# Optimization experiments

Measured on AMD Instinct MI355X. Metric: run time of the kernel, lower is better.

The kernel has to match this reference:

```python
import math
import jax, jax.numpy as jnp
import numpy as np

HEAD_DIM = 128
SKETCH_DIM = 256  # multiple of 8, no padding needed in pack
_BIT_WEIGHTS = jnp.array([1, 2, 4, 8, 16, 32, 64, 128], dtype=jnp.uint8)


def _pack_bits(bits):
    # bits: uint8 0/1, trailing dim = SKETCH_DIM (multiple of 8)
    *lead, d = bits.shape
    b = bits.reshape(*lead, d // 8, 8)
    return (b * _BIT_WEIGHTS).sum(axis=-1).astype(jnp.uint8)


def _unpack_bits(packed, out_dim):
    # packed: uint8 [..., n] -> float32 [..., out_dim] of 0/1
    shifts = jnp.arange(8, dtype=jnp.uint8)
    bits = (packed[..., None] >> shifts) & jnp.uint8(1)
    bits = bits.reshape(*packed.shape[:-1], -1)[..., :out_dim]
    return bits.astype(jnp.float32)


def setup_inputs() -> dict:
    key = jax.random.key(0)
    kq, kk, kg = jax.random.split(key, 3)
    q = jax.random.normal(kq, (4, 32, 16, HEAD_DIM), dtype=jnp.float32)
    k = jax.random.normal(kk, (4, 32, 8192, HEAD_DIM), dtype=jnp.float32)
    G = jax.random.normal(kg, (HEAD_DIM, SKETCH_DIM), dtype=jnp.float32) / math.sqrt(SKETCH_DIM)
    return {"q": q, "k": k, "G": G}


def reference(q, k, G):
    # project_query: q @ G -> [B, H, Q, sketch_dim]
    q_sketch = jnp.einsum('bhqd,ds->bhqs', q, G)
    # sketch_key: sign-quantize k @ G, pack into uint8
    proj = jnp.einsum('bhkd,ds->bhks', k, G)
    bits = (proj > 0).astype(jnp.uint8)
    k_packed = _pack_bits(bits)  # [B, H, K, sketch_dim//8] uint8
    # estimate_scores: unpack to +/-1, dequant matmul, unbiasing scale
    k_signs = _unpack_bits(k_packed, SKETCH_DIM) * 2.0 - 1.0
    est = jnp.einsum('bhqs,bhks->bhqk', q_sketch, k_signs.astype(q_sketch.dtype))
    return est * jnp.float32(math.sqrt(math.pi / 2))
```

## Files before the change

### kernel.cpp

```cpp
#include <hip/hip_runtime.h>
#include <math.h>

typedef _Float16 f16;
typedef _Float16 f16x4 __attribute__((ext_vector_type(4)));
typedef _Float16 f16x8 __attribute__((ext_vector_type(8)));
typedef float    f32x4 __attribute__((ext_vector_type(4)));
typedef unsigned int u32;
typedef unsigned long long u64;

#define NHEADS 128
#define KLEN   8192
#define DDIM   128
#define SDIM   256
#define NROWS  (NHEADS * KLEN)
#define SCALE  1.2533141373155003f
#define TAU    2e-5f

#define QS_OFF     0
#define GFH_OFF    (1u << 20)
#define GFL_OFF    ((1u << 20) + (64u << 10))
#define GT_OFF     ((1u << 20) + (128u << 10))
#define PACKED_OFF (2u << 20)

__device__ __forceinline__ float seq_dot_np(const float* __restrict__ a,
                                            const float* __restrict__ gcol) {
  float acc = 0.0f;
  #pragma unroll 8
  for (int d = 0; d < DDIM; ++d)
    acc = __builtin_fmaf(a[d], gcol[d], acc);
  return acc;
}

__global__ void prep_qs_kernel(const float* __restrict__ q,
                               const float* __restrict__ G,
                               f16* __restrict__ qs16) {
  int idx = blockIdx.x * 256 + threadIdx.x;
  int s  = idx & 255;
  int hq = idx >> 8;
  const float* qr = q + (size_t)hq * DDIM;
  float acc = 0.f;
  #pragma unroll 8
  for (int d = 0; d < DDIM; ++d) acc += qr[d] * G[d * SDIM + s];
  qs16[idx] = (f16)acc;
}

__global__ void prep_g_kernel(const float* __restrict__ G,
                              f16* __restrict__ gfh, f16* __restrict__ gfl,
                              float* __restrict__ gt) {
  int t = blockIdx.x * 256 + threadIdx.x;
  int tl   = t >> 8;
  int c    = (t >> 6) & 3;
  int lane = t & 63;
  int s  = tl * 16 + (lane & 15);
  int d0 = c * 32 + (lane >> 4) * 8;
  f16x8 hh, ll;
  #pragma unroll
  for (int j = 0; j < 8; ++j) {
    float g = G[(size_t)(d0 + j) * SDIM + s];
    f16 h = (f16)g;
    hh[j] = h;
    ll[j] = (f16)((g - (float)h) * 4096.0f);
    gt[(size_t)s * DDIM + d0 + j] = g;
  }
  *(f16x8*)(gfh + (size_t)t * 8) = hh;
  *(f16x8*)(gfl + (size_t)t * 8) = ll;
}

__launch_bounds__(512, 1)
__global__ void proj_sign_kernel(const float* __restrict__ kmat,
                                 const f16* __restrict__ gfh,
                                 const f16* __restrict__ gfl,
                                 u32* __restrict__ packed,
                                 u32* __restrict__ smask) {
  __shared__ __align__(16) f16 lds[2][4][64][8];

  const int tid  = threadIdx.x;
  const int lane = tid & 63;
  const int w    = tid >> 6;
  const int g4 = lane >> 4;
  const int ln = lane & 15;
  const size_t rowbase = (size_t)blockIdx.x * 256;

  f16x8 Gh[2][4], Gl[2][4];
  #pragma unroll
  for (int mt = 0; mt < 2; ++mt)
    #pragma unroll
    for (int kc = 0; kc < 4; ++kc) {
      size_t o = ((size_t)((w * 2 + mt) * 4 + kc) * 64 + lane) * 8;
      Gh[mt][kc] = *(const f16x8*)(gfh + o);
      Gl[mt][kc] = *(const f16x8*)(gfl + o);
    }

  const int srl = tid >> 5;
  const int sd0 = (tid & 31) * 4;
  const int skc = sd0 >> 5;
  const int slf = srl | (((sd0 >> 3) & 3) << 4);
  const int sj0 = sd0 & 7;

  float4 rv = *(const float4*)(kmat + (rowbase + srl) * DDIM + sd0);

  for (int t = 0; t < 16; ++t) {
    f16x4 h4, l4;
    {
      float vv0 = rv.x, vv1 = rv.y, vv2 = rv.z, vv3 = rv.w;
      f16 h;
      h = (f16)vv0; h4[0] = h; l4[0] = (f16)((vv0 - (float)h) * 4096.0f);
      h = (f16)vv1; h4[1] = h; l4[1] = (f16)((vv1 - (float)h) * 4096.0f);
      h = (f16)vv2; h4[2] = h; l4[2] = (f16)((vv2 - (float)h) * 4096.0f);
      h = (f16)vv3; h4[3] = h; l4[3] = (f16)((vv3 - (float)h) * 4096.0f);
    }
    float4 rn;
    if (t < 15)
      rn = *(const float4*)(kmat + (rowbase + (size_t)(t + 1) * 16 + srl) * DDIM + sd0);
    *(f16x4*)&lds[0][skc][slf][sj0] = h4;
    *(f16x4*)&lds[1][skc][slf][sj0] = l4;
    __syncthreads();

    f32x4 ah0 = {0,0,0,0}, aa0 = {0,0,0,0}, ab0 = {0,0,0,0};
    f32x4 ah1 = {0,0,0,0}, aa1 = {0,0,0,0}, ab1 = {0,0,0,0};
    #pragma unroll
    for (int kc = 0; kc < 4; ++kc) {
      f16x8 Bh = *(const f16x8*)&lds[0][kc][lane][0];
      f16x8 Bl = *(const f16x8*)&lds[1][kc][lane][0];
      ah0 = __builtin_amdgcn_mfma_f32_16x16x32_f16(Gh[0][kc], Bh, ah0, 0, 0, 0);
      aa0 = __builtin_amdgcn_mfma_f32_16x16x32_f16(Gh[0][kc], Bl, aa0, 0, 0, 0);
      ab0 = __builtin_amdgcn_mfma_f32_16x16x32_f16(Gl[0][kc], Bh, ab0, 0, 0, 0);
      ah1 = __builtin_amdgcn_mfma_f32_16x16x32_f16(Gh[1][kc], Bh, ah1, 0, 0, 0);
      aa1 = __builtin_amdgcn_mfma_f32_16x16x32_f16(Gh[1][kc], Bl, aa1, 0, 0, 0);
      ab1 = __builtin_amdgcn_mfma_f32_16x16x32_f16(Gl[1][kc], Bh, ab1, 0, 0, 0);
    }
    float p[2][4];
    #pragma unroll
    for (int r = 0; r < 4; ++r) {
      p[0][r] = ah0[r] + (aa0[r] + ab0[r]) * 2.44140625e-4f;
      p[1][r] = ah1[r] + (aa1[r] + ab1[r]) * 2.44140625e-4f;
    }

    u32 pbits = 0, sbits = 0;
    #pragma unroll
    for (int mt = 0; mt < 2; ++mt)
      #pragma unroll
      for (int r = 0; r < 4; ++r)
        if (p[mt][r] > 0.0f) pbits |= (1u << (mt * 16 + g4 * 4 + r));
    float mn = __builtin_fabsf(p[0][0]);
    #pragma unroll
    for (int mt = 0; mt < 2; ++mt)
      #pragma unroll
      for (int r = 0; r < 4; ++r)
        mn = fminf(mn, __builtin_fabsf(p[mt][r]));
    if (__any(mn < TAU ? 1 : 0)) {
      #pragma unroll
      for (int mt = 0; mt < 2; ++mt)
        #pragma unroll
        for (int r = 0; r < 4; ++r)
          if (__builtin_fabsf(p[mt][r]) < TAU) sbits |= (1u << (mt * 16 + g4 * 4 + r));
    }
    pbits |= __shfl_xor(pbits, 16);  pbits |= __shfl_xor(pbits, 32);
    sbits |= __shfl_xor(sbits, 16);  sbits |= __shfl_xor(sbits, 32);
    if (lane < 16) {
      size_t row = rowbase + (size_t)t * 16 + ln;
      packed[row * 8 + w] = pbits;
      smask [row * 8 + w] = sbits;
    }
    __syncthreads();
    if (t < 15) rv = rn;
  }
}

__global__ void fixup_kernel(const float* __restrict__ kmat,
                             const float* __restrict__ gt,
                             u32* __restrict__ packed,
                             const u32* __restrict__ smask) {
  int row = blockIdx.x * 256 + threadIdx.x;
  if (row >= NROWS) return;
  const u32* mp = smask + (size_t)row * 8;
  uint4 m0 = *(const uint4*)mp;
  uint4 m1 = *(const uint4*)(mp + 4);
  u32 mw[8] = {m0.x, m0.y, m0.z, m0.w, m1.x, m1.y, m1.z, m1.w};
  if (!(mw[0] | mw[1] | mw[2] | mw[3] | mw[4] | mw[5] | mw[6] | mw[7])) return;
  const float* a = kmat + (size_t)row * DDIM;
  #pragma unroll
  for (int wd = 0; wd < 8; ++wd) {
    u32 m = mw[wd];
    if (!m) continue;
    u32 pk = packed[(size_t)row * 8 + wd];
    while (m) {
      int b = __ffs(m) - 1;  m &= m - 1;
      int s = wd * 32 + b;
      float acc = seq_dot_np(a, gt + (size_t)s * DDIM);
      if (acc > 0.0f) pk |= (1u << b);
      else            pk &= ~(1u << b);
    }
    packed[(size_t)row * 8 + wd] = pk;
  }
}

__launch_bounds__(256)
__global__ void est_kernel(const f16* __restrict__ qs16,
                           const u32* __restrict__ packed,
                           float* __restrict__ out) {
  const int tid  = threadIdx.x;
  const int lane = tid & 63;
  const int w    = tid >> 6;
  const int wg   = blockIdx.x;
  const int head   = wg >> 5;
  const int kchunk = (wg & 31) * 256;
  const int g4 = lane >> 4, ln = lane & 15;

  f16x8 aq[8];
  const f16* qb = qs16 + (size_t)head * 16 * SDIM;
  #pragma unroll
  for (int c = 0; c < 8; ++c)
    aq[c] = *(const f16x8*)(qb + ln * SDIM + c * 32 + g4 * 8);

  const int kb = kchunk + w * 64;
  #pragma unroll
  for (int kt = 0; kt < 4; ++kt) {
    int krow = kb + kt * 16 + ln;
    const u32* bp = packed + (size_t)(head * KLEN + krow) * 8;
    uint4 q0 = *(const uint4*)bp;
    uint4 q1 = *(const uint4*)(bp + 4);
    u32 b32[8] = {q0.x, q0.y, q0.z, q0.w, q1.x, q1.y, q1.z, q1.w};
    f32x4 acc = {0, 0, 0, 0};
    #pragma unroll
    for (int c = 0; c < 8; ++c) {
      u32 byte8 = (b32[c] >> (8 * g4)) & 0xffu;
      union { u32 u[4]; f16x8 h; } sv;
      #pragma unroll
      for (int pp = 0; pp < 4; ++pp) {
        u32 v = 0x3C003C00u;
        v |= ((byte8 >> (2 * pp))     & 1u) ? 0u : 0x8000u;
        v |= ((byte8 >> (2 * pp + 1)) & 1u) ? 0u : 0x80000000u;
        sv.u[pp] = v;
      }
      acc = __builtin_amdgcn_mfma_f32_16x16x32_f16(aq[c], sv.h, acc, 0, 0, 0);
    }
    float* ob = out + (size_t)(head * 16) * KLEN + kb + kt * 16 + ln;
    #pragma unroll
    for (int r = 0; r < 4; ++r) {
      int qrow = g4 * 4 + r;
      ob[(size_t)qrow * KLEN] = acc[r] * SCALE;
    }
  }
}

extern "C" void kernel_launch(void* const* d_in, const int* in_sizes, int n_in,
                              void* d_out, int out_size, void* d_ws, size_t ws_size,
                              hipStream_t stream) {
  const float* q = (const float*)d_in[0];
  const float* k = (const float*)d_in[1];
  const float* G = (const float*)d_in[2];
  float* out = (float*)d_out;
  char* ws = (char*)d_ws;

  f16*   qs16   = (f16*)(ws + QS_OFF);
  f16*   gfh    = (f16*)(ws + GFH_OFF);
  f16*   gfl    = (f16*)(ws + GFL_OFF);
  float* gt     = (float*)(ws + GT_OFF);
  u32*   packed = (u32*)(ws + PACKED_OFF);

  u32* smask = (u32*)d_out;

  prep_qs_kernel<<<2048, 256, 0, stream>>>(q, G, qs16);
  prep_g_kernel<<<16, 256, 0, stream>>>(G, gfh, gfl, gt);
  proj_sign_kernel<<<4096, 512, 0, stream>>>(k, gfh, gfl, packed, smask);
  fixup_kernel<<<4096, 256, 0, stream>>>(k, gt, packed, smask);
  est_kernel<<<4096, 256, 0, stream>>>(qs16, packed, out);
}
```

Before: 307.9 us.

## Switch sign-projection kernel to 32x32x16 MFMA with 32-row tiles

Replaces the 16x16x32 MFMA tiling in the projection/sign kernel with 32x32x16 MFMAs, so each wave covers 32 sketch columns by 32 key rows per step and the loop runs 8 iterations instead of 16. G fragments are re-laid-out in the prep kernel to match, and LDS staging, the bit packing and the shuffle reduction are rewritten for the new accumulator layout. The intent is fewer MFMA instructions, fewer barriers and fewer iterations per block. The cost is larger accumulators, which raises register pressure, and a more intricate lane-to-row mapping for the bits.

```diff
diff --git a/kernel.cpp b/kernel.cpp
--- a/kernel.cpp
+++ b/kernel.cpp
@@ -5,6 +5,7 @@
 typedef _Float16 f16x4 __attribute__((ext_vector_type(4)));
 typedef _Float16 f16x8 __attribute__((ext_vector_type(8)));
 typedef float    f32x4 __attribute__((ext_vector_type(4)));
+typedef float    f32x16 __attribute__((ext_vector_type(16)));
 typedef unsigned int u32;
 typedef unsigned long long u64;
 
@@ -48,11 +49,11 @@
                               f16* __restrict__ gfh, f16* __restrict__ gfl,
                               float* __restrict__ gt) {
   int t = blockIdx.x * 256 + threadIdx.x;
-  int tl   = t >> 8;
-  int c    = (t >> 6) & 3;
+  int w    = t >> 9;
+  int kc   = (t >> 6) & 7;
   int lane = t & 63;
-  int s  = tl * 16 + (lane & 15);
-  int d0 = c * 32 + (lane >> 4) * 8;
+  int s  = w * 32 + (lane & 31);
+  int d0 = kc * 16 + (lane >> 5) * 8;
   f16x8 hh, ll;
   #pragma unroll
   for (int j = 0; j < 8; ++j) {
@@ -72,98 +73,99 @@
                                  const f16* __restrict__ gfl,
                                  u32* __restrict__ packed,
                                  u32* __restrict__ smask) {
-  __shared__ __align__(16) f16 lds[2][4][64][8];
+  __shared__ __align__(16) f16 lds[2][8][64][8];
 
   const int tid  = threadIdx.x;
   const int lane = tid & 63;
   const int w    = tid >> 6;
-  const int g4 = lane >> 4;
-  const int ln = lane & 15;
+  const int l5 = lane >> 5;
   const size_t rowbase = (size_t)blockIdx.x * 256;
 
-  f16x8 Gh[2][4], Gl[2][4];
-  #pragma unroll
-  for (int mt = 0; mt < 2; ++mt)
-    #pragma unroll
-    for (int kc = 0; kc < 4; ++kc) {
-      size_t o = ((size_t)((w * 2 + mt) * 4 + kc) * 64 + lane) * 8;
-      Gh[mt][kc] = *(const f16x8*)(gfh + o);
-      Gl[mt][kc] = *(const f16x8*)(gfl + o);
-    }
+  f16x8 Gh[8], Gl[8];
+  #pragma unroll
+  for (int kc = 0; kc < 8; ++kc) {
+    size_t o = ((size_t)(w * 8 + kc) * 64 + lane) * 8;
+    Gh[kc] = *(const f16x8*)(gfh + o);
+    Gl[kc] = *(const f16x8*)(gfl + o);
+  }
 
   const int srl = tid >> 5;
   const int sd0 = (tid & 31) * 4;
-  const int skc = sd0 >> 5;
-  const int slf = srl | (((sd0 >> 3) & 3) << 4);
+  const int skc = sd0 >> 4;
+  const int slot = ((sd0 >> 3) & 1) * 32;
   const int sj0 = sd0 & 7;
-
-  float4 rv = *(const float4*)(kmat + (rowbase + srl) * DDIM + sd0);
-
-  for (int t = 0; t < 16; ++t) {
-    f16x4 h4, l4;
+  const float* kp0 = kmat + (rowbase + srl) * DDIM + sd0;
+
+  float4 rv0 = *(const float4*)kp0;
+  float4 rv1 = *(const float4*)(kp0 + (size_t)16 * DDIM);
+
+  for (int t = 0; t < 8; ++t) {
     {
-      float vv0 = rv.x, vv1 = rv.y, vv2 = rv.z, vv3 = rv.w;
       f16 h;
-      h = (f16)vv0; h4[0] = h; l4[0] = (f16)((vv0 - (float)h) * 4096.0f);
-      h = (f16)vv1; h4[1] = h; l4[1] = (f16)((vv1 - (float)h) * 4096.0f);
-      h = (f16)vv2; h4[2] = h; l4[2] = (f16)((vv2 - (float)h) * 4096.0f);
-      h = (f16)vv3; h4[3] = h; l4[3] = (f16)((vv3 - (float)h) * 4096.0f);
-    }
-    float4 rn;
-    if (t < 15)
-      rn = *(const float4*)(kmat + (rowbase + (size_t)(t + 1) * 16 + srl) * DDIM + sd0);
-    *(f16x4*)&lds[0][skc][slf][sj0] = h4;
-    *(f16x4*)&lds[1][skc][slf][sj0] = l4;
+      f16x4 h4, l4;
+      h = (f16)rv0.x; h4[0] = h; l4[0] = (f16)((rv0.x - (float)h) * 4096.0f);
+      h = (f16)rv0.y; h4[1] = h; l4[1] = (f16)((rv0.y - (float)h) * 4096.0f);
+      h = (f16)rv0.z; h4[2] = h; l4[2] = (f16)((rv0.z - (float)h) * 4096.0f);
+      h = (f16)rv0.w; h4[3] = h; l4[3] = (f16)((rv0.w - (float)h) * 4096.0f);
+      *(f16x4*)&lds[0][skc][slot + srl][sj0] = h4;
+      *(f16x4*)&lds[1][skc][slot + srl][sj0] = l4;
+      h = (f16)rv1.x; h4[0] = h; l4[0] = (f16)((rv1.x - (float)h) * 4096.0f);
+      h = (f16)rv1.y; h4[1] = h; l4[1] = (f16)((rv1.y - (float)h) * 4096.0f);
+      h = (f16)rv1.z; h4[2] = h; l4[2] = (f16)((rv1.z - (float)h) * 4096.0f);
+      h = (f16)rv1.w; h4[3] = h; l4[3] = (f16)((rv1.w - (float)h) * 4096.0f);
+      *(f16x4*)&lds[0][skc][slot + srl + 16][sj0] = h4;
+      *(f16x4*)&lds[1][skc][slot + srl + 16][sj0] = l4;
+    }
+    float4 rn0, rn1;
+    if (t < 7) {
+      const float* np_ = kp0 + (size_t)(t + 1) * 32 * DDIM;
+      rn0 = *(const float4*)np_;
+      rn1 = *(const float4*)(np_ + (size_t)16 * DDIM);
+    }
     __syncthreads();
 
-    f32x4 ah0 = {0,0,0,0}, aa0 = {0,0,0,0}, ab0 = {0,0,0,0};
-    f32x4 ah1 = {0,0,0,0}, aa1 = {0,0,0,0}, ab1 = {0,0,0,0};
-    #pragma unroll
-    for (int kc = 0; kc < 4; ++kc) {
+    f32x16 ch = {0,0,0,0,0,0,0,0,0,0,0,0,0,0,0,0};
+    f32x16 ca = {0,0,0,0,0,0,0,0,0,0,0,0,0,0,0,0};
+    f32x16 cb = {0,0,0,0,0,0,0,0,0,0,0,0,0,0,0,0};
+    #pragma unroll
+    for (int kc = 0; kc < 8; ++kc) {
       f16x8 Bh = *(const f16x8*)&lds[0][kc][lane][0];
       f16x8 Bl = *(const f16x8*)&lds[1][kc][lane][0];
-      ah0 = __builtin_amdgcn_mfma_f32_16x16x32_f16(Gh[0][kc], Bh, ah0, 0, 0, 0);
-      aa0 = __builtin_amdgcn_mfma_f32_16x16x32_f16(Gh[0][kc], Bl, aa0, 0, 0, 0);
-      ab0 = __builtin_amdgcn_mfma_f32_16x16x32_f16(Gl[0][kc], Bh, ab0, 0, 0, 0);
-      ah1 = __builtin_amdgcn_mfma_f32_16x16x32_f16(Gh[1][kc], Bh, ah1, 0, 0, 0);
-      aa1 = __builtin_amdgcn_mfma_f32_16x16x32_f16(Gh[1][kc], Bl, aa1, 0, 0, 0);
-      ab1 = __builtin_amdgcn_mfma_f32_16x16x32_f16(Gl[1][kc], Bh, ab1, 0, 0, 0);
-    }
-    float p[2][4];
-    #pragma unroll
-    for (int r = 0; r < 4; ++r) {
-      p[0][r] = ah0[r] + (aa0[r] + ab0[r]) * 2.44140625e-4f;
-      p[1][r] = ah1[r] + (aa1[r] + ab1[r]) * 2.44140625e-4f;
-    }
+      ch = __builtin_amdgcn_mfma_f32_32x32x16_f16(Gh[kc], Bh, ch, 0, 0, 0);
+      ca = __builtin_amdgcn_mfma_f32_32x32x16_f16(Gh[kc], Bl, ca, 0, 0, 0);
+      cb = __builtin_amdgcn_mfma_f32_32x32x16_f16(Gl[kc], Bh, cb, 0, 0, 0);
+    }
+    float p[16];
+    #pragma unroll
+    for (int r = 0; r < 16; ++r)
+      p[r] = ch[r] + (ca[r] + cb[r]) * 2.44140625e-4f;
 
     u32 pbits = 0, sbits = 0;
     #pragma unroll
-    for (int mt = 0; mt < 2; ++mt)
-      #pragma unroll
-      for (int r = 0; r < 4; ++r)
-        if (p[mt][r] > 0.0f) pbits |= (1u << (mt * 16 + g4 * 4 + r));
-    float mn = __builtin_fabsf(p[0][0]);
-    #pragma unroll
-    for (int mt = 0; mt < 2; ++mt)
-      #pragma unroll
-      for (int r = 0; r < 4; ++r)
-        mn = fminf(mn, __builtin_fabsf(p[mt][r]));
+    for (int r = 0; r < 16; ++r) {
+      int srow = (r & 3) + 8 * (r >> 2) + 4 * l5;
+      if (p[r] > 0.0f) pbits |= (1u << srow);
+    }
+    float mn = __builtin_fabsf(p[0]);
+    #pragma unroll
+    for (int r = 1; r < 16; ++r)
+      mn = fminf(mn, __builtin_fabsf(p[r]));
     if (__any(mn < TAU ? 1 : 0)) {
       #pragma unroll
-      for (int mt = 0; mt < 2; ++mt)
-        #pragma unroll
-        for (int r = 0; r < 4; ++r)
-          if (__builtin_fabsf(p[mt][r]) < TAU) sbits |= (1u << (mt * 16 + g4 * 4 + r));
-    }
-    pbits |= __shfl_xor(pbits, 16);  pbits |= __shfl_xor(pbits, 32);
-    sbits |= __shfl_xor(sbits, 16);  sbits |= __shfl_xor(sbits, 32);
-    if (lane < 16) {
-      size_t row = rowbase + (size_t)t * 16 + ln;
+      for (int r = 0; r < 16; ++r) {
+        int srow = (r & 3) + 8 * (r >> 2) + 4 * l5;
+        if (__builtin_fabsf(p[r]) < TAU) sbits |= (1u << srow);
+      }
+    }
+    pbits |= __shfl_xor(pbits, 32);
+    sbits |= __shfl_xor(sbits, 32);
+    if (lane < 32) {
+      size_t row = rowbase + (size_t)t * 32 + lane;
       packed[row * 8 + w] = pbits;
       smask [row * 8 + w] = sbits;
     }
     __syncthreads();
-    if (t < 15) rv = rn;
+    if (t < 7) { rv0 = rn0; rv1 = rn1; }
   }
 }
 
```

Result: slower. 347.7 us (+12.9%).
